# Performance work log

Measured on AMD Instinct MI355X. Metric: run time of the kernel, lower is better.

The kernel has to match this reference:

```python
import jax, jax.numpy as jnp
import numpy as np

SIDES, LAYERS, NH = 2, 2, 2
DEPTH, B = 7, 8
NPT = (3 ** DEPTH - 1) // 2  # 1093 nodes per perfect ternary tree
N = B * NPT                  # 8744
E, H = 256, 512
NUM_USERS, NUM_POIS, NUM_CATS, NUM_COOS, TMAX = 2000, 5000, 300, 50, 600
FUSE = NUM_POIS + NUM_CATS + NUM_COOS


def setup_inputs() -> dict:
    key = jax.random.key(0)
    cnt = [0]
    def nk():
        cnt[0] += 1
        return jax.random.fold_in(key, cnt[0])
    def rn(*s):
        return jax.random.normal(nk(), s, jnp.float32) * 0.02
    inp = dict(
        user_ids=jax.random.randint(nk(), (SIDES, N), 0, NUM_USERS, jnp.int32),
        feat_ids=jax.random.randint(nk(), (SIDES, N), 0, FUSE, jnp.int32),
        time_ids=jax.random.randint(nk(), (SIDES, N), 0, TMAX, jnp.int32),
        mask=jnp.ones((SIDES, N), jnp.int32),
        depth=DEPTH, n_trees=B,
        user_emb=rn(SIDES, NUM_USERS, 128), fuse_emb=rn(SIDES, FUSE, 128),
        time_pe=rn(SIDES, TMAX, E),
        Wf=rn(SIDES, H, E), bf=jnp.zeros((SIDES, H)),
        Wiou=rn(SIDES, 3 * H, E), Uiou=rn(SIDES, 3 * H, 3 * H), biou=jnp.zeros((SIDES, 3 * H)),
        attn_in_w=rn(SIDES, LAYERS, 3 * H, H), attn_in_b=jnp.zeros((SIDES, LAYERS, 3 * H)),
        attn_out_w=rn(SIDES, LAYERS, H, H), attn_out_b=jnp.zeros((SIDES, LAYERS, H)),
        ff1_w=rn(SIDES, LAYERS, H, H), ff1_b=jnp.zeros((SIDES, LAYERS, H)),
        ff2_w=rn(SIDES, LAYERS, H, H), ff2_b=jnp.zeros((SIDES, LAYERS, H)),
        ln1_w=jnp.ones((SIDES, LAYERS, H)), ln1_b=jnp.zeros((SIDES, LAYERS, H)),
        ln2_w=jnp.ones((SIDES, LAYERS, H)), ln2_b=jnp.zeros((SIDES, LAYERS, H)),
        dec_poi_w=rn(SIDES, NUM_POIS, H), dec_poi_b=jnp.zeros((SIDES, NUM_POIS)),
        dec_cat_w=rn(SIDES, NUM_CATS, H), dec_cat_b=jnp.zeros((SIDES, NUM_CATS)),
        dec_coo_w=rn(SIDES, NUM_COOS, H), dec_coo_b=jnp.zeros((SIDES, NUM_COOS)),
        cat2poi_w=rn(SIDES, NUM_POIS, NUM_CATS), cat2poi_b=jnp.zeros((SIDES, NUM_POIS)),
        coo2poi_w=rn(SIDES, NUM_POIS, NUM_COOS), coo2poi_b=jnp.zeros((SIDES, NUM_POIS)),
        mtl=jnp.ones((SIDES, 3)),
        c0=(jax.random.uniform(nk(), (SIDES, N, H), jnp.float32) * 2.0 - 1.0) * 0.025,
    )
    return inp


def _ln(x, w, b, eps=1e-5):
    m = x.mean(-1, keepdims=True)
    v = ((x - m) ** 2).mean(-1, keepdims=True)
    return (x - m) / jnp.sqrt(v + eps) * w + b


def _mha(x, iw, ib, ow, ob):
    M, S, Hd = x.shape
    q, k, v = jnp.split(x @ iw.T + ib, 3, -1)
    hd = Hd // NH
    def rs(t):
        return t.reshape(M, S, NH, hd).transpose(0, 2, 1, 3)
    q, k, v = rs(q), rs(k), rs(v)
    att = jax.nn.softmax((q * (hd ** -0.5)) @ k.transpose(0, 1, 3, 2), -1)
    o = (att @ v).transpose(0, 2, 1, 3).reshape(M, S, Hd)
    return o @ ow.T + ob


def _enc(x, iw, ib, ow, ob, f1w, f1b, f2w, f2b, l1w, l1b, l2w, l2b):
    # post-norm TransformerEncoderLayer, relu, eval mode (no dropout)
    x = _ln(x + _mha(x, iw, ib, ow, ob), l1w, l1b)
    return _ln(x + (jax.nn.relu(x @ f1w.T + f1b) @ f2w.T + f2b), l2w, l2b)


def _forward(user_ids, feat_ids, time_ids, mask, depth, n_trees,
             user_emb, fuse_emb, time_pe, Wf, bf, Wiou, Uiou, biou,
             attn_in_w, attn_in_b, attn_out_w, attn_out_b,
             ff1_w, ff1_b, ff2_w, ff2_b, ln1_w, ln1_b, ln2_w, ln2_b,
             dec_poi_w, dec_poi_b, dec_cat_w, dec_cat_b, dec_coo_w, dec_coo_b,
             cat2poi_w, cat2poi_b, coo2poi_w, coo2poi_b, mtl, c0):
    Hd = Wf.shape[1]
    npt = (3 ** depth - 1) // 2
    Bt = n_trees
    offs = [(3 ** l - 1) // 2 for l in range(depth)]
    outs = []
    for s in range(SIDES):
        m = mask[s]
        uid, fid, tid = user_ids[s] * m, feat_ids[s] * m, time_ids[s] * m
        emb = jnp.concatenate([user_emb[s][uid], fuse_emb[s][fid]], -1) + 0.5 * time_pe[s][tid]
        mf = m.astype(emb.dtype)[:, None]
        x = (emb * mf).reshape(Bt, npt, -1)              # masked node features
        iou0 = ((emb @ Wiou[s].T) * mf).reshape(Bt, npt, 3 * Hd)  # leaf iou init
        c0s = c0[s].reshape(Bt, npt, Hd)
        h = jnp.zeros((Bt, npt, Hd), emb.dtype)
        c = jnp.zeros((Bt, npt, Hd), emb.dtype)
        for l in range(depth - 1, -1, -1):  # bottom-up topo propagation, level-major layout
            st, n = offs[l], 3 ** l
            if l == depth - 1:  # leaves: no reduce, apply with initial iou and c
                iou = iou0[:, st:st + n]
                cpre = c0s[:, st:st + n]
            else:
                cs = offs[l + 1]
                hch = h[:, cs:cs + 3 * n].reshape(Bt * n, 3, Hd)   # mailbox h_child
                cch = c[:, cs:cs + 3 * n].reshape(Bt, n, 3, Hd)    # mailbox c_child
                z = hch
                for L in range(LAYERS):
                    z = _enc(z, attn_in_w[s, L], attn_in_b[s, L], attn_out_w[s, L], attn_out_b[s, L],
                             ff1_w[s, L], ff1_b[s, L], ff2_w[s, L], ff2_b[s, L],
                             ln1_w[s, L], ln1_b[s, L], ln2_w[s, L], ln2_b[s, L])
                hc = z.reshape(Bt, n, 3 * Hd)
                xl = x[:, st:st + n]
                Wx = xl @ Wf[s].T
                f = jax.nn.sigmoid(jnp.concatenate([Wx] * 3, -1) + hc + jnp.tile(bf[s], 3))
                iou = xl @ Wiou[s].T + hc @ Uiou[s].T + biou[s]
                cpre = jnp.sum(f.reshape(Bt, n, 3, Hd) * cch, axis=2)
            i, o, u = jnp.split(iou, 3, -1)
            cn = jax.nn.sigmoid(i) * jnp.tanh(u) + cpre
            hn = jax.nn.sigmoid(o) * jnp.tanh(cn)
            h = h.at[:, st:st + n].set(hn)
            c = c.at[:, st:st + n].set(cn)
        hN = h.reshape(-1, Hd)
        poi = hN @ dec_poi_w[s].T + dec_poi_b[s]
        cat = hN @ dec_cat_w[s].T + dec_cat_b[s]
        coo = hN @ dec_coo_w[s].T + dec_coo_b[s]
        p = mtl[s]
        poi_mt = (0.5 * jnp.exp(-p[0]) * poi + p[0]
                  + 0.5 * jnp.exp(-p[1]) * (cat @ cat2poi_w[s].T + cat2poi_b[s]) + p[1]
                  + 0.5 * jnp.exp(-p[2]) * (coo @ coo2poi_w[s].T + coo2poi_b[s]) + p[2])
        outs += [poi_mt, cat, coo]
    return tuple(outs)


def reference(user_ids, feat_ids, time_ids, mask, depth, n_trees,
              user_emb, fuse_emb, time_pe, Wf, bf, Wiou, Uiou, biou,
              attn_in_w, attn_in_b, attn_out_w, attn_out_b,
              ff1_w, ff1_b, ff2_w, ff2_b, ln1_w, ln1_b, ln2_w, ln2_b,
              dec_poi_w, dec_poi_b, dec_cat_w, dec_cat_b, dec_coo_w, dec_coo_b,
              cat2poi_w, cat2poi_b, coo2poi_w, coo2poi_b, mtl, c0):
    return _forward(user_ids, feat_ids, time_ids, mask, depth, n_trees,
                    user_emb, fuse_emb, time_pe, Wf, bf, Wiou, Uiou, biou,
                    attn_in_w, attn_in_b, attn_out_w, attn_out_b,
                    ff1_w, ff1_b, ff2_w, ff2_b, ln1_w, ln1_b, ln2_w, ln2_b,
                    dec_poi_w, dec_poi_b, dec_cat_w, dec_cat_b, dec_coo_w, dec_coo_b,
                    cat2poi_w, cat2poi_b, coo2poi_w, coo2poi_b, mtl, c0)
```

## Files before the change

### kernel.cpp

```cpp
#include <hip/hip_runtime.h>
#include <math.h>

#define SIDES 2
#define LAYERS 2
#define NTREE 8
#define NPT 1093
#define NN (NTREE*NPT)
#define EE 256
#define HH 512
#define NUSERS 2000
#define NPOI 5000
#define NCAT 300
#define NCOO 50
#define FUSEN 5350
#define TMAXN 600
#define TOKMAX 5832
#define PARMAX 1944

constexpr long OUT_S   = 46780400L;
constexpr long CAT_OFF = 43720000L;
constexpr long COO_OFF = 46343200L;

constexpr long H_S    = (long)NN*HH;
constexpr long X_S    = (long)NN*EE;
constexpr long Z_S    = (long)TOKMAX*HH;
constexpr long QKV_S  = (long)TOKMAX*3*HH;
constexpr long WXI_S  = (long)PARMAX*2048;
constexpr long WEFF_S = (long)NPOI*HH;

typedef __attribute__((ext_vector_type(8))) short  bf16x8;
typedef __attribute__((ext_vector_type(8))) ushort u16x8;
typedef __attribute__((ext_vector_type(4))) ushort u16x4;
typedef __attribute__((ext_vector_type(4))) float  f32x4;

__device__ __forceinline__ float sigm(float x){ return 1.f/(1.f+expf(-x)); }
__device__ __forceinline__ ushort f2b(float f){
  union { float f; unsigned u; } v; v.f = f;
  return (ushort)((v.u + 0x7fffu + ((v.u >> 16) & 1u)) >> 16);
}
__device__ __forceinline__ float b2f(ushort u){
  union { unsigned u; float f; } v; v.u = (unsigned)u << 16; return v.f;
}

constexpr int PB_EMB  = 2*NN;
constexpr int PB_MCVT = 6494;
constexpr int PB_WCOMB= 2*2048;
constexpr int PB_BCOMB= 16;
constexpr int PB_POI  = 2*5000;
constexpr int PB_TP   = 2*512;
constexpr int PB_WEI  = 2*2500;
constexpr int PB_BEF  = 40;
constexpr int PB_TOT  = PB_EMB+PB_MCVT+PB_WCOMB+PB_BCOMB+PB_POI+PB_TP+PB_WEI+PB_BEF;

__global__ void __launch_bounds__(256) prep_k(
    const int* __restrict__ uid, const int* __restrict__ fid,
    const int* __restrict__ tids, const int* __restrict__ mask,
    const float* __restrict__ uemb, const float* __restrict__ femb,
    const float* __restrict__ tpe, ushort* __restrict__ X,
    ushort* ainW, const float* attn_in_w, ushort* aoutW, const float* attn_out_w,
    ushort* f1W, const float* ff1_w, ushort* f2W, const float* ff2_w,
    ushort* dcatW, const float* dec_cat_w, ushort* dcooW, const float* dec_coo_w,
    ushort* wcomb, const float* Wf, const float* Wiou, const float* Uiou,
    float* bcomb, const float* biou,
    ushort* c2pB, const float* cat2poi_w, ushort* o2pB, const float* coo2poi_w,
    ushort* dctT, ushort* dcoT,
    ushort* weffB, const float* dec_poi_w, const float* mtl,
    float* beff, const float* dec_poi_b, const float* dec_cat_b,
    const float* cat2poi_b, const float* dec_coo_b, const float* coo2poi_b){
  int b = blockIdx.x;
  int tid = threadIdx.x;
  if (b < PB_EMB){
    int s = b / NN; long i = b - s*NN; int d = tid;
    int m = mask[(long)s*NN + i];
    int u = uid[(long)s*NN + i]*m, f = fid[(long)s*NN + i]*m, t = tids[(long)s*NN + i]*m;
    float e = (d < 128) ? uemb[((long)s*NUSERS + u)*128 + d]
                        : femb[((long)s*FUSEN + f)*128 + (d-128)];
    e += 0.5f * tpe[((long)s*TMAXN + t)*256 + d];
    X[(long)s*X_S + i*EE + d] = f2b(e * (float)m);
    return;
  }
  b -= PB_EMB;
  if (b < PB_MCVT){
    const long n0 = 3145728, n1 = 1048576, n2 = 1048576, n3 = 1048576,
               n4 = 307200, n5 = 51200;
    long i = ((long)b*256 + tid)*4;
    ushort* d; const float* s; long off;
    if      (i < n0){ d=ainW;  s=attn_in_w;  off=i; }
    else if ((i-=n0) < n1){ d=aoutW; s=attn_out_w; off=i; }
    else if ((i-=n1) < n2){ d=f1W;  s=ff1_w;  off=i; }
    else if ((i-=n2) < n3){ d=f2W;  s=ff2_w;  off=i; }
    else if ((i-=n3) < n4){ d=dcatW; s=dec_cat_w; off=i; }
    else if ((i-=n4) < n5){ d=dcooW; s=dec_coo_w; off=i; }
    else return;
    f32x4 v = *(const f32x4*)(s + off);
    *(u16x4*)(d + off) = (u16x4){f2b(v[0]), f2b(v[1]), f2b(v[2]), f2b(v[3])};
    return;
  }
  b -= PB_MCVT;
  if (b < PB_WCOMB){
    int s = b >> 11; int row = b & 2047;
    ushort* dst = wcomb + (long)s*2048*1792 + (long)row*1792;
    for (int col = tid; col < 1792; col += 256){
      float v;
      if (row < 512) v = (col < 256) ? Wf[((long)s*512 + row)*256 + col] : 0.f;
      else {
        int r = row - 512;
        v = (col < 256) ? Wiou[((long)s*1536 + r)*256 + col]
                        : Uiou[((long)s*1536 + r)*1536 + (col-256)];
      }
      dst[col] = f2b(v);
    }
    return;
  }
  b -= PB_WCOMB;
  if (b < PB_BCOMB){
    int s = b >> 3; int c = (b & 7)*256 + tid;
    bcomb[(long)s*2048 + c] = (c < 512) ? 0.f : biou[(long)s*1536 + (c-512)];
    return;
  }
  b -= PB_BCOMB;
  if (b < PB_POI){
    int s = b / 5000; int r = b - s*5000;
    for (int c = tid; c < 320; c += 256){
      float v = (c < 300) ? cat2poi_w[((long)s*5000 + r)*300 + c] : 0.f;
      c2pB[((long)s*5000 + r)*320 + c] = f2b(v);
    }
    if (tid < 64){
      float v = (tid < 50) ? coo2poi_w[((long)s*5000 + r)*50 + tid] : 0.f;
      o2pB[((long)s*5000 + r)*64 + tid] = f2b(v);
    }
    return;
  }
  b -= PB_POI;
  if (b < PB_TP){
    int s = b >> 9; int h = b & 511;
    for (int c = tid; c < 320; c += 256){
      float v = (c < 300) ? dec_cat_w[((long)s*300 + c)*512 + h] : 0.f;
      dctT[((long)s*512 + h)*320 + c] = f2b(v);
    }
    if (tid < 64){
      float v = (tid < 50) ? dec_coo_w[((long)s*50 + tid)*512 + h] : 0.f;
      dcoT[((long)s*512 + h)*64 + tid] = f2b(v);
    }
    return;
  }
  b -= PB_TP;
  if (b < PB_WEI){
    int s = b / 2500; int blk = b - s*2500;
    long i = ((long)blk*256 + tid)*4;
    float a0 = 0.5f*expf(-mtl[(long)s*3]);
    f32x4 v = *(const f32x4*)(dec_poi_w + (long)s*WEFF_S + i);
    *(u16x4*)(weffB + (long)s*WEFF_S + i) =
        (u16x4){f2b(a0*v[0]), f2b(a0*v[1]), f2b(a0*v[2]), f2b(a0*v[3])};
    return;
  }
  b -= PB_WEI;
  {
    int s = b / 20; int n = (b - s*20)*256 + tid;
    if (n >= NPOI) return;
    const float* mt = mtl + (long)s*3;
    float a0 = 0.5f*expf(-mt[0]), a1 = 0.5f*expf(-mt[1]), a2 = 0.5f*expf(-mt[2]);
    float acc1 = 0.f, acc2 = 0.f;
    for (int c = 0; c < NCAT; c++)
      acc1 += dec_cat_b[(long)s*NCAT + c] * cat2poi_w[((long)s*NPOI + n)*NCAT + c];
    for (int c = 0; c < NCOO; c++)
      acc2 += dec_coo_b[(long)s*NCOO + c] * coo2poi_w[((long)s*NPOI + n)*NCOO + c];
    beff[(long)s*NPOI + n] = a0*dec_poi_b[(long)s*NPOI + n]
        + a1*(acc1 + cat2poi_b[(long)s*NPOI + n]) + a2*(acc2 + coo2poi_b[(long)s*NPOI + n])
        + mt[0] + mt[1] + mt[2];
  }
}

template<int MODE, bool OBF>
__global__ void __launch_bounds__(256)
mgemm_k(const ushort* __restrict__ A1, long lda1, long sA1,
        const ushort* __restrict__ A2, long lda2, long sA2,
        int kSplit, int mapN, int mapOff,
        const ushort* __restrict__ Wt, long ldw, long sW,
        const float* __restrict__ bias, long sB,
        void* __restrict__ Cv, long ldc, long sC,
        int M, int Nc, int K, int nbx,
        const float* __restrict__ mtl, int mtlIdx){
  int s = blockIdx.z;
  A1 += (long)s*sA1; A2 += (long)s*sA2; Wt += (long)s*sW;
  if (bias) bias += (long)s*sB;

  int flat = blockIdx.x, nwg = gridDim.x;
  int xcd = flat & 7, q = nwg >> 3, r8 = nwg & 7;
  int nf = (xcd < r8 ? xcd*(q+1) : r8*(q+1) + (xcd - r8)*q) + (flat >> 3);
  int bx = nf % nbx, by = nf / nbx;
  int m0 = by*128, n0 = bx*128;

  __shared__ ushort As[128*64];
  __shared__ ushort Ws[128*64];

  int tid = threadIdx.x;
  int lane = tid & 63, wave = tid >> 6;
  int wr = wave >> 1, wc = wave & 1;
  int fr = lane & 15, kc = lane >> 4;

  int baseRow = tid >> 3;
  int c16 = tid & 7;
  int col8 = c16*8;
  int swz = (baseRow & 7) << 4;

  long gA1[4], gA2[4], gW[4];
  int wbyte[4];
  #pragma unroll
  for (int c = 0; c < 4; c++){
    int row = baseRow + c*32;
    int ra = m0 + row; if (ra > M-1) ra = M-1;
    gA2[c] = ra;
    if (mapN > 0){ int tr = ra / mapN; gA1[c] = (long)(tr*NPT + mapOff + (ra - tr*mapN)); }
    else gA1[c] = ra;
    int rw = n0 + row; if (rw > Nc-1) rw = Nc-1;
    gW[c] = rw;
    wbyte[c] = row*128 + ((c16*16) ^ swz);
  }

  u16x8 rA[4], rW[4];
  {
    bool u1 = (0 < kSplit);
    const ushort* asrc = u1 ? A1 : A2;
    long ld = u1 ? lda1 : lda2;
    const long* g = u1 ? gA1 : gA2;
    #pragma unroll
    for (int c = 0; c < 4; c++){
      rA[c] = *(const u16x8*)(asrc + g[c]*ld + col8);
      rW[c] = *(const u16x8*)(Wt + gW[c]*ldw + col8);
    }
  }

  f32x4 acc[4][4];
  #pragma unroll
  for (int i = 0; i < 4; i++)
    #pragma unroll
    for (int j = 0; j < 4; j++) acc[i][j] = (f32x4){0.f,0.f,0.f,0.f};

  for (int k0 = 0; k0 < K; k0 += 64){
    #pragma unroll
    for (int c = 0; c < 4; c++){
      *(u16x8*)((char*)As + wbyte[c]) = rA[c];
      *(u16x8*)((char*)Ws + wbyte[c]) = rW[c];
    }
    __syncthreads();
    int kn = k0 + 64;
    if (kn < K){
      bool u1 = (kn < kSplit);
      const ushort* asrc = u1 ? A1 : A2;
      long ld = u1 ? lda1 : lda2;
      const long* g = u1 ? gA1 : gA2;
      long colb = u1 ? (long)kn : (long)(kn - kSplit);
      #pragma unroll
      for (int c = 0; c < 4; c++){
        rA[c] = *(const u16x8*)(asrc + g[c]*ld + colb + col8);
        rW[c] = *(const u16x8*)(Wt + gW[c]*ldw + kn + col8);
      }
    }
    #pragma unroll
    for (int h = 0; h < 2; h++){
      bf16x8 af[4], bw[4];
      #pragma unroll
      for (int i = 0; i < 4; i++){
        int row = wr*64 + i*16 + fr;
        int byo = row*128 + ((h*64 + kc*16) ^ ((row & 7) << 4));
        af[i] = *(const bf16x8*)((const char*)As + byo);
      }
      #pragma unroll
      for (int j = 0; j < 4; j++){
        int row = wc*64 + j*16 + fr;
        int byo = row*128 + ((h*64 + kc*16) ^ ((row & 7) << 4));
        bw[j] = *(const bf16x8*)((const char*)Ws + byo);
      }
      #pragma unroll
      for (int i = 0; i < 4; i++)
        #pragma unroll
        for (int j = 0; j < 4; j++)
          acc[i][j] = __builtin_amdgcn_mfma_f32_16x16x32_bf16(bw[j], af[i], acc[i][j], 0, 0, 0);
    }
    __syncthreads();
  }

  float alpha = 1.f;
  if (MODE == 4) alpha = 0.5f*expf(-mtl[(long)s*3 + mtlIdx]);
  int ccol = lane & 15, cr4 = (lane >> 4)*4;
  bool vecN = ((Nc & 3) == 0);
  float* Cf = (float*)Cv + (long)s*sC;
  ushort* Cb = (ushort*)Cv + (long)s*sC;
  #pragma unroll
  for (int i = 0; i < 4; i++){
    int gm = m0 + wr*64 + i*16 + ccol;
    if (gm >= M) continue;
    long rowoff = (long)gm*ldc;
    #pragma unroll
    for (int j = 0; j < 4; j++){
      int gn0 = n0 + wc*64 + j*16 + cr4;
      if (gn0 >= Nc) continue;
      f32x4 v = acc[i][j];
      if (MODE != 4 && bias){ f32x4 bv = *(const f32x4*)&bias[gn0]; v += bv; }
      if (MODE == 1){ v = (f32x4){fmaxf(v[0],0.f),fmaxf(v[1],0.f),fmaxf(v[2],0.f),fmaxf(v[3],0.f)}; }
      if (OBF){
        u16x4* cp = (u16x4*)&Cb[rowoff + gn0];
        if (MODE == 4){
          u16x4 o = *cp;
          *cp = (u16x4){f2b(b2f(o[0]) + alpha*v[0]), f2b(b2f(o[1]) + alpha*v[1]),
                        f2b(b2f(o[2]) + alpha*v[2]), f2b(b2f(o[3]) + alpha*v[3])};
        } else {
          *cp = (u16x4){f2b(v[0]), f2b(v[1]), f2b(v[2]), f2b(v[3])};
        }
      } else {
        if (vecN){
          f32x4* cp = (f32x4*)&Cf[rowoff + gn0];
          if (MODE == 4){ f32x4 o = *cp; *cp = o + alpha*v; }
          else *cp = v;
        } else {
          #pragma unroll
          for (int r = 0; r < 4; r++){
            int gn = gn0 + r; if (gn >= Nc) continue;
            if (MODE == 4) Cf[rowoff + gn] += alpha*v[r];
            else Cf[rowoff + gn] = v[r];
          }
        }
      }
    }
  }
}

__global__ void __launch_bounds__(256) attn_k(const ushort* __restrict__ qkv,
                                              ushort* __restrict__ o){
  int s = blockIdx.z;
  int w = threadIdx.x >> 6, lane = threadIdx.x & 63;
  int seq = blockIdx.x*2 + (w >> 1);
  int h = w & 1;
  const ushort* base = qkv + (long)s*QKV_S + (long)seq*3*1536 + h*256 + lane*4;
  float q[3][4], k[3][4], v[3][4];
  #pragma unroll
  for (int i = 0; i < 3; i++){
    u16x4 tq = *(const u16x4*)(base + (long)i*1536);
    u16x4 tk = *(const u16x4*)(base + (long)i*1536 + 512);
    u16x4 tv = *(const u16x4*)(base + (long)i*1536 + 1024);
    #pragma unroll
    for (int e = 0; e < 4; e++){ q[i][e]=b2f(tq[e]); k[i][e]=b2f(tk[e]); v[i][e]=b2f(tv[e]); }
  }
  float p[9];
  #pragma unroll
  for (int i = 0; i < 3; i++)
    #pragma unroll
    for (int j = 0; j < 3; j++){
      float acc = 0.f;
      #pragma unroll
      for (int e = 0; e < 4; e++) acc += q[i][e]*k[j][e];
      p[i*3+j] = acc;
    }
  #pragma unroll
  for (int m = 1; m < 64; m <<= 1)
    #pragma unroll
    for (int t = 0; t < 9; t++) p[t] += __shfl_xor(p[t], m);
  float att[9];
  #pragma unroll
  for (int i = 0; i < 3; i++){
    float a = p[i*3]*0.0625f, bb = p[i*3+1]*0.0625f, c = p[i*3+2]*0.0625f;
    float mx = fmaxf(a, fmaxf(bb, c));
    a = expf(a-mx); bb = expf(bb-mx); c = expf(c-mx);
    float inv = 1.f/(a+bb+c);
    att[i*3] = a*inv; att[i*3+1] = bb*inv; att[i*3+2] = c*inv;
  }
  ushort* ob = o + (long)s*Z_S + (long)seq*1536 + h*256 + lane*4;
  #pragma unroll
  for (int i = 0; i < 3; i++){
    u16x4 r;
    #pragma unroll
    for (int e = 0; e < 4; e++)
      r[e] = f2b(att[i*3]*v[0][e] + att[i*3+1]*v[1][e] + att[i*3+2]*v[2][e]);
    *(u16x4*)(ob + (long)i*512) = r;
  }
}

__global__ void __launch_bounds__(256) add_ln_k(ushort* __restrict__ zout, long sZ,
                         const ushort* __restrict__ res, long sR, int mapN, int mapOff,
                         const ushort* __restrict__ tb, long sT,
                         const float* __restrict__ w, const float* __restrict__ b,
                         long wstr){
  int s = blockIdx.z;
  int wv = threadIdx.x >> 6, lane = threadIdx.x & 63;
  int r = blockIdx.x*4 + wv;
  int g = r;
  if (mapN > 0){ int tr = r / mapN; g = tr*NPT + mapOff + (r - tr*mapN); }
  int d0 = lane*8;
  u16x8 rr = *(const u16x8*)(res + (long)s*sR + (long)g*HH + d0);
  u16x8 tt = *(const u16x8*)(tb  + (long)s*sT + (long)r*HH + d0);
  float x[8];
  float sum = 0.f;
  #pragma unroll
  for (int e = 0; e < 8; e++){ x[e] = b2f(rr[e]) + b2f(tt[e]); sum += x[e]; }
  #pragma unroll
  for (int m = 1; m < 64; m <<= 1) sum += __shfl_xor(sum, m);
  float mean = sum * (1.f/512.f);
  float vs = 0.f;
  #pragma unroll
  for (int e = 0; e < 8; e++){ float d = x[e]-mean; vs += d*d; }
  #pragma unroll
  for (int m = 1; m < 64; m <<= 1) vs += __shfl_xor(vs, m);
  float inv = 1.f/sqrtf(vs*(1.f/512.f) + 1e-5f);
  const float* wr_ = w + (long)s*wstr + d0;
  const float* br_ = b + (long)s*wstr + d0;
  f32x4 w0 = *(const f32x4*)wr_, w1 = *(const f32x4*)(wr_+4);
  f32x4 b0 = *(const f32x4*)br_, b1 = *(const f32x4*)(br_+4);
  u16x8 ov;
  #pragma unroll
  for (int e = 0; e < 4; e++){
    ov[e]   = f2b((x[e]-mean)*inv*w0[e] + b0[e]);
    ov[e+4] = f2b((x[e+4]-mean)*inv*w1[e] + b1[e]);
  }
  *(u16x8*)(zout + (long)s*sZ + (long)r*HH + d0) = ov;
}

__global__ void leaf_k(const ushort* __restrict__ iou, const float* __restrict__ c0,
                       ushort* __restrict__ hbuf, float* __restrict__ cbuf){
  int s = blockIdx.z, p = blockIdx.x;
  int tree = p / 729, j = p - tree*729;
  long row = (long)(tree*NPT + 364 + j)*HH;
  const ushort* iour = iou + (long)s*QKV_S + (long)p*1536;
  const float* c0r = c0 + (long)s*H_S + row;
  for (int d = threadIdx.x; d < HH; d += 256){
    float cn = sigm(b2f(iour[d])) * tanhf(b2f(iour[1024 + d])) + c0r[d];
    float hn = sigm(b2f(iour[512 + d])) * tanhf(cn);
    hbuf[(long)s*H_S + row + d] = f2b(hn);
    cbuf[(long)s*H_S + row + d] = cn;
  }
}

__global__ void combine_k(const ushort* __restrict__ wxiou, const ushort* __restrict__ z,
                          const float* __restrict__ bfv, const float* __restrict__ cbuf,
                          ushort* __restrict__ hbuf, float* __restrict__ cout,
                          int n, int st, int cs){
  int s = blockIdx.z, p = blockIdx.x;
  int tree = p / n, j = p - tree*n;
  const ushort* wr_ = wxiou + (long)s*WXI_S + (long)p*2048;
  const ushort* zr  = z + (long)s*Z_S + (long)p*1536;
  const float* bfr  = bfv + (long)s*HH;
  const float* cch  = cbuf + (long)s*H_S + (long)(tree*NPT + cs + 3*j)*HH;
  long orow = (long)s*H_S + (long)(tree*NPT + st + j)*HH;
  for (int d = threadIdx.x; d < HH; d += 256){
    float wv = b2f(wr_[d]) + bfr[d];
    float cpre = 0.f;
    #pragma unroll
    for (int ch = 0; ch < 3; ch++){
      float fg = sigm(wv + b2f(zr[ch*512 + d]));
      cpre += fg * cch[ch*512 + d];
    }
    float iv = b2f(wr_[512 + d]), ov = b2f(wr_[1024 + d]), uv = b2f(wr_[1536 + d]);
    float cn = sigm(iv)*tanhf(uv) + cpre;
    float hn = sigm(ov)*tanhf(cn);
    hbuf[orow + d] = f2b(hn);
    cout[orow + d] = cn;
  }
}

#define GEMM(MODE, OBF, A1, LDA1, SA1, A2, LDA2, SA2, KSPL, MAPN, MAPOFF, WT, LDW, SW, \
             BI, SB, CC, LDC, SC, M, NC, K)                                            \
  do { int nbx_ = ((NC)+127)/128, nby_ = ((M)+127)/128;                                \
    mgemm_k<MODE, OBF><<<dim3(nbx_*nby_, 1, SIDES), 256, 0, stream>>>(                 \
      A1, LDA1, SA1, A2, LDA2, SA2, KSPL, MAPN, MAPOFF, WT, LDW, SW, BI, SB,           \
      CC, LDC, SC, M, NC, K, nbx_, mtl, 0); } while(0)
#define GEMM4(OBF, A1, LDA1, SA1, WT, LDW, SW, CC, LDC, SC, M, NC, K, IDX)             \
  do { int nbx_ = ((NC)+127)/128, nby_ = ((M)+127)/128;                                \
    mgemm_k<4, OBF><<<dim3(nbx_*nby_, 1, SIDES), 256, 0, stream>>>(                    \
      A1, LDA1, SA1, A1, LDA1, SA1, K, 0, 0, WT, LDW, SW, (const float*)nullptr, 0L,   \
      CC, LDC, SC, M, NC, K, nbx_, mtl, IDX); } while(0)

extern "C" void kernel_launch(void* const* d_in, const int* in_sizes, int n_in,
                              void* d_out, int out_size, void* d_ws, size_t ws_size,
                              hipStream_t stream){
  (void)in_sizes; (void)n_in; (void)out_size; (void)ws_size;
  const int*   user_ids  = (const int*)d_in[0];
  const int*   feat_ids  = (const int*)d_in[1];
  const int*   time_ids  = (const int*)d_in[2];
  const int*   mask      = (const int*)d_in[3];
  const float* user_emb  = (const float*)d_in[6];
  const float* fuse_emb  = (const float*)d_in[7];
  const float* time_pe   = (const float*)d_in[8];
  const float* Wf        = (const float*)d_in[9];
  const float* bf        = (const float*)d_in[10];
  const float* Wiou      = (const float*)d_in[11];
  const float* Uiou      = (const float*)d_in[12];
  const float* biou      = (const float*)d_in[13];
  const float* attn_in_w = (const float*)d_in[14];
  const float* attn_in_b = (const float*)d_in[15];
  const float* attn_out_w= (const float*)d_in[16];
  const float* attn_out_b= (const float*)d_in[17];
  const float* ff1_w     = (const float*)d_in[18];
  const float* ff1_b     = (const float*)d_in[19];
  const float* ff2_w     = (const float*)d_in[20];
  const float* ff2_b     = (const float*)d_in[21];
  const float* ln1_w     = (const float*)d_in[22];
  const float* ln1_b     = (const float*)d_in[23];
  const float* ln2_w     = (const float*)d_in[24];
  const float* ln2_b     = (const float*)d_in[25];
  const float* dec_poi_w = (const float*)d_in[26];
  const float* dec_poi_b = (const float*)d_in[27];
  const float* dec_cat_w = (const float*)d_in[28];
  const float* dec_cat_b = (const float*)d_in[29];
  const float* dec_coo_w = (const float*)d_in[30];
  const float* dec_coo_b = (const float*)d_in[31];
  const float* cat2poi_w = (const float*)d_in[32];
  const float* cat2poi_b = (const float*)d_in[33];
  const float* coo2poi_w = (const float*)d_in[34];
  const float* coo2poi_b = (const float*)d_in[35];
  const float* mtl       = (const float*)d_in[36];
  const float* c0        = (const float*)d_in[37];

  float* out = (float*)d_out;

  ushort* wsu = (ushort*)d_ws;
  ushort* Hb    = wsu;
  ushort* ainW  = Hb    + 2*H_S;
  ushort* aoutW = ainW  + (long)2*2*1536*512;
  ushort* f1W   = aoutW + (long)2*2*512*512;
  ushort* f2W   = f1W   + (long)2*2*512*512;
  ushort* wcomb = f2W   + (long)2*2*512*512;
  ushort* dcatW = wcomb + (long)2*2048*1792;
  ushort* dcooW = dcatW + (long)2*300*512;
  ushort* weffB = dcooW + (long)2*50*512;
  float*  bcomb = (float*)(weffB + (long)2*WEFF_S);
  float*  beff  = bcomb + 2*2048;

  float*  Cb   = out + OUT_S;
  ushort* osu  = (ushort*)(Cb + 2*H_S);
  ushort* QKV  = osu;
  ushort* Zb   = QKV  + 2*QKV_S;
  ushort* TMP  = Zb   + 2*Z_S;
  ushort* WXI  = TMP  + 2*Z_S;
  ushort* Xb   = WXI  + 2*WXI_S;
  ushort* c2pB = Xb   + 2*X_S;
  ushort* o2pB = c2pB + (long)2*5000*320;
  ushort* dctT = o2pB + (long)2*5000*64;
  ushort* dcoT = dctT + (long)2*512*320;

  prep_k<<<dim3(PB_TOT), 256, 0, stream>>>(
      user_ids, feat_ids, time_ids, mask, user_emb, fuse_emb, time_pe, Xb,
      ainW, attn_in_w, aoutW, attn_out_w, f1W, ff1_w, f2W, ff2_w,
      dcatW, dec_cat_w, dcooW, dec_coo_w,
      wcomb, Wf, Wiou, Uiou, bcomb, biou,
      c2pB, cat2poi_w, o2pB, coo2poi_w, dctT, dcoT,
      weffB, dec_poi_w, mtl,
      beff, dec_poi_b, dec_cat_b, cat2poi_b, dec_coo_b, coo2poi_b);

  GEMM(0, true, Xb, 256L, X_S, Xb, 256L, X_S, 256, 729, 364,
       wcomb + (long)512*1792, 1792L, (long)2048*1792,
       (const float*)nullptr, 0L, QKV, 1536L, QKV_S, 5832, 1536, 256);
  leaf_k<<<dim3(5832, 1, SIDES), 256, 0, stream>>>(QKV, c0, Hb, Cb);

  const int p3[7]   = {1,3,9,27,81,243,729};
  const int offs[7] = {0,1,4,13,40,121,364};

  for (int l = 5; l >= 0; l--){
    int n = p3[l], st = offs[l], cs = offs[l+1];
    int P = NTREE*n, T = 3*P;
    for (int L = 0; L < LAYERS; L++){
      const ushort* zin = (L == 0) ? Hb : Zb;
      long zld = 512, zs = (L == 0) ? H_S : Z_S;
      int mN = (L == 0) ? 3*n : 0, mO = (L == 0) ? cs : 0;
      GEMM(0, true, zin, zld, zs, zin, zld, zs, 512, mN, mO,
           ainW + (long)L*1536*512, 512L, (long)2*1536*512,
           attn_in_b + (long)L*1536, (long)LAYERS*1536, QKV, 1536L, QKV_S, T, 1536, 512);
      attn_k<<<dim3(P/2, 1, SIDES), 256, 0, stream>>>(QKV, TMP);
      GEMM(0, true, TMP, 512L, Z_S, TMP, 512L, Z_S, 512, 0, 0,
           aoutW + (long)L*512*512, 512L, (long)2*512*512,
           attn_out_b + (long)L*512, (long)LAYERS*512, QKV, 512L, QKV_S, T, 512, 512);
      add_ln_k<<<dim3(T/4, 1, SIDES), 256, 0, stream>>>(Zb, Z_S, zin, zs, mN, mO,
           QKV, QKV_S, ln1_w + (long)L*512, ln1_b + (long)L*512, (long)LAYERS*512);
      GEMM(1, true, Zb, 512L, Z_S, Zb, 512L, Z_S, 512, 0, 0,
           f1W + (long)L*512*512, 512L, (long)2*512*512,
           ff1_b + (long)L*512, (long)LAYERS*512, TMP, 512L, Z_S, T, 512, 512);
      GEMM(0, true, TMP, 512L, Z_S, TMP, 512L, Z_S, 512, 0, 0,
           f2W + (long)L*512*512, 512L, (long)2*512*512,
           ff2_b + (long)L*512, (long)LAYERS*512, QKV, 512L, QKV_S, T, 512, 512);
      add_ln_k<<<dim3(T/4, 1, SIDES), 256, 0, stream>>>(Zb, Z_S, Zb, Z_S, 0, 0,
           QKV, QKV_S, ln2_w + (long)L*512, ln2_b + (long)L*512, (long)LAYERS*512);
    }
    GEMM(0, true, Xb, 256L, X_S, Zb, 1536L, Z_S, 256, n, st,
         wcomb, 1792L, (long)2048*1792, bcomb, 2048L, WXI, 2048L, WXI_S, P, 2048, 1792);
    combine_k<<<dim3(P, 1, SIDES), 256, 0, stream>>>(WXI, Zb, bf, Cb, Hb, Cb, n, st, cs);
  }

  GEMM(0, false, Hb, 512L, H_S, Hb, 512L, H_S, 512, 0, 0,
       dcatW, 512L, (long)NCAT*512, dec_cat_b, (long)NCAT,
       out + CAT_OFF, (long)NCAT, OUT_S, NN, NCAT, 512);
  GEMM(0, false, Hb, 512L, H_S, Hb, 512L, H_S, 512, 0, 0,
       dcooW, 512L, (long)NCOO*512, dec_coo_b, (long)NCOO,
       out + COO_OFF, (long)NCOO, OUT_S, NN, NCOO, 512);

  GEMM4(true, c2pB, 320L, (long)5000*320, dctT, 320L, (long)512*320,
        weffB, 512L, WEFF_S, 5000, 512, 320, 1);
  GEMM4(true, o2pB, 64L, (long)5000*64, dcoT, 64L, (long)512*64,
        weffB, 512L, WEFF_S, 5000, 512, 64, 2);

  GEMM(0, false, Hb, 512L, H_S, Hb, 512L, H_S, 512, 0, 0,
       weffB, 512L, WEFF_S, beff, (long)NPOI,
       out, (long)NPOI, OUT_S, NN, NPOI, 512);
}
```

Baseline: 1.560 ms.

## Fuse output GEMM with residual LayerNorm for small levels; merge decoder weight-fold GEMMs

Adds a gemmln_k kernel that computes a 64-row x 512-column GEMM tile, adds bias and residual, and applies LayerNorm in shared memory. It replaces the attention-out and FF2 GEMM plus add_ln_k pairs when the token count is small (T<=648). This removes a launch and a round trip through global memory at the small tree levels that are bound by launch count and latency. Separately, the two MODE-4 accumulate GEMMs that fold cat2poi/coo2poi into the POI decoder weights become one K-concatenated GEMM, with the mtl scale pre-applied during prep. The fused kernel runs few blocks and uses a large shared-memory footprint, which limits parallelism.

```diff
diff --git a/kernel.cpp b/kernel.cpp
--- a/kernel.cpp
+++ b/kernel.cpp
@@ -63,7 +63,7 @@
     ushort* wcomb, const float* Wf, const float* Wiou, const float* Uiou,
     float* bcomb, const float* biou,
     ushort* c2pB, const float* cat2poi_w, ushort* o2pB, const float* coo2poi_w,
-    ushort* dctT, ushort* dcoT,
+    ushort* dcT2,
     ushort* weffB, const float* dec_poi_w, const float* mtl,
     float* beff, const float* dec_poi_b, const float* dec_cat_b,
     const float* cat2poi_b, const float* dec_coo_b, const float* coo2poi_b){
@@ -121,12 +121,14 @@
   b -= PB_BCOMB;
   if (b < PB_POI){
     int s = b / 5000; int r = b - s*5000;
+    float a1 = 0.5f*expf(-mtl[(long)s*3 + 1]);
+    float a2 = 0.5f*expf(-mtl[(long)s*3 + 2]);
     for (int c = tid; c < 320; c += 256){
-      float v = (c < 300) ? cat2poi_w[((long)s*5000 + r)*300 + c] : 0.f;
+      float v = (c < 300) ? a1*cat2poi_w[((long)s*5000 + r)*300 + c] : 0.f;
       c2pB[((long)s*5000 + r)*320 + c] = f2b(v);
     }
     if (tid < 64){
-      float v = (tid < 50) ? coo2poi_w[((long)s*5000 + r)*50 + tid] : 0.f;
+      float v = (tid < 50) ? a2*coo2poi_w[((long)s*5000 + r)*50 + tid] : 0.f;
       o2pB[((long)s*5000 + r)*64 + tid] = f2b(v);
     }
     return;
@@ -134,13 +136,12 @@
   b -= PB_POI;
   if (b < PB_TP){
     int s = b >> 9; int h = b & 511;
-    for (int c = tid; c < 320; c += 256){
-      float v = (c < 300) ? dec_cat_w[((long)s*300 + c)*512 + h] : 0.f;
-      dctT[((long)s*512 + h)*320 + c] = f2b(v);
-    }
-    if (tid < 64){
-      float v = (tid < 50) ? dec_coo_w[((long)s*50 + tid)*512 + h] : 0.f;
-      dcoT[((long)s*512 + h)*64 + tid] = f2b(v);
+    ushort* dst = dcT2 + ((long)s*512 + h)*384;
+    for (int c = tid; c < 384; c += 256){
+      float v = 0.f;
+      if (c < 300)                 v = dec_cat_w[((long)s*300 + c)*512 + h];
+      else if (c >= 320 && c < 370) v = dec_coo_w[((long)s*50 + (c-320))*512 + h];
+      dst[c] = f2b(v);
     }
     return;
   }
@@ -297,14 +298,15 @@
       int gn0 = n0 + wc*64 + j*16 + cr4;
       if (gn0 >= Nc) continue;
       f32x4 v = acc[i][j];
-      if (MODE != 4 && bias){ f32x4 bv = *(const f32x4*)&bias[gn0]; v += bv; }
+      if (MODE != 4 && MODE != 2 && bias){ f32x4 bv = *(const f32x4*)&bias[gn0]; v += bv; }
       if (MODE == 1){ v = (f32x4){fmaxf(v[0],0.f),fmaxf(v[1],0.f),fmaxf(v[2],0.f),fmaxf(v[3],0.f)}; }
       if (OBF){
         u16x4* cp = (u16x4*)&Cb[rowoff + gn0];
-        if (MODE == 4){
+        if (MODE == 4 || MODE == 2){
           u16x4 o = *cp;
-          *cp = (u16x4){f2b(b2f(o[0]) + alpha*v[0]), f2b(b2f(o[1]) + alpha*v[1]),
-                        f2b(b2f(o[2]) + alpha*v[2]), f2b(b2f(o[3]) + alpha*v[3])};
+          float a = (MODE == 4) ? alpha : 1.f;
+          *cp = (u16x4){f2b(b2f(o[0]) + a*v[0]), f2b(b2f(o[1]) + a*v[1]),
+                        f2b(b2f(o[2]) + a*v[2]), f2b(b2f(o[3]) + a*v[3])};
         } else {
           *cp = (u16x4){f2b(v[0]), f2b(v[1]), f2b(v[2]), f2b(v[3])};
         }
@@ -312,16 +314,171 @@
         if (vecN){
           f32x4* cp = (f32x4*)&Cf[rowoff + gn0];
           if (MODE == 4){ f32x4 o = *cp; *cp = o + alpha*v; }
+          else if (MODE == 2){ f32x4 o = *cp; *cp = o + v; }
           else *cp = v;
         } else {
           #pragma unroll
           for (int r = 0; r < 4; r++){
             int gn = gn0 + r; if (gn >= Nc) continue;
             if (MODE == 4) Cf[rowoff + gn] += alpha*v[r];
+            else if (MODE == 2) Cf[rowoff + gn] += v[r];
             else Cf[rowoff + gn] = v[r];
           }
         }
       }
+    }
+  }
+}
+
+__global__ void __launch_bounds__(256)
+gemmln_k(const ushort* __restrict__ A, long sA,
+         const ushort* __restrict__ res, long sR, int mapN, int mapOff,
+         const ushort* __restrict__ Wt, long sW,
+         const float* __restrict__ bias, long sB,
+         const float* __restrict__ lnw, const float* __restrict__ lnb, long wstr,
+         ushort* __restrict__ Zo, long sZ, int M){
+  int s = blockIdx.z;
+  A += (long)s*sA; res += (long)s*sR; Wt += (long)s*sW;
+  bias += (long)s*sB; lnw += (long)s*wstr; lnb += (long)s*wstr;
+  ushort* Z = Zo + (long)s*sZ;
+  int m0 = blockIdx.x*64;
+
+  __shared__ ushort As[64*64];
+  __shared__ ushort Ws[128*64];
+  __shared__ ushort zs[64*512];
+  __shared__ float ssum[64], ssq[64];
+
+  int tid = threadIdx.x;
+  int lane = tid & 63, wave = tid >> 6;
+  int wr = wave >> 1, wc = wave & 1;
+  int fr = lane & 15, kc = lane >> 4;
+  int ccol = lane & 15, cr4 = (lane >> 4)*4;
+
+  int baseRow = tid >> 3;
+  int c16 = tid & 7;
+  int col8 = c16*8;
+
+  long gA[2]; int abyte[2];
+  #pragma unroll
+  for (int c = 0; c < 2; c++){
+    int row = baseRow + c*32;
+    int ra = m0 + row; if (ra > M-1) ra = M-1;
+    gA[c] = ra;
+    abyte[c] = row*128 + ((c16*16) ^ ((row & 7) << 4));
+  }
+  int wbyte[4];
+  #pragma unroll
+  for (int c = 0; c < 4; c++){
+    int row = baseRow + c*32;
+    wbyte[c] = row*128 + ((c16*16) ^ ((row & 7) << 4));
+  }
+
+  float psum[2] = {0.f, 0.f}, psq[2] = {0.f, 0.f};
+
+  for (int nt = 0; nt < 4; nt++){
+    f32x4 acc[2][4];
+    #pragma unroll
+    for (int i = 0; i < 2; i++)
+      #pragma unroll
+      for (int j = 0; j < 4; j++) acc[i][j] = (f32x4){0.f,0.f,0.f,0.f};
+    for (int k0 = 0; k0 < 512; k0 += 64){
+      #pragma unroll
+      for (int c = 0; c < 2; c++)
+        *(u16x8*)((char*)As + abyte[c]) = *(const u16x8*)(A + gA[c]*512 + k0 + col8);
+      #pragma unroll
+      for (int c = 0; c < 4; c++){
+        int rw = nt*128 + baseRow + c*32;
+        *(u16x8*)((char*)Ws + wbyte[c]) = *(const u16x8*)(Wt + (long)rw*512 + k0 + col8);
+      }
+      __syncthreads();
+      #pragma unroll
+      for (int h = 0; h < 2; h++){
+        bf16x8 af[2], bw[4];
+        #pragma unroll
+        for (int i = 0; i < 2; i++){
+          int row = wr*32 + i*16 + fr;
+          int byo = row*128 + ((h*64 + kc*16) ^ ((row & 7) << 4));
+          af[i] = *(const bf16x8*)((const char*)As + byo);
+        }
+        #pragma unroll
+        for (int j = 0; j < 4; j++){
+          int row = wc*64 + j*16 + fr;
+          int byo = row*128 + ((h*64 + kc*16) ^ ((row & 7) << 4));
+          bw[j] = *(const bf16x8*)((const char*)Ws + byo);
+        }
+        #pragma unroll
+        for (int i = 0; i < 2; i++)
+          #pragma unroll
+          for (int j = 0; j < 4; j++)
+            acc[i][j] = __builtin_amdgcn_mfma_f32_16x16x32_bf16(bw[j], af[i], acc[i][j], 0, 0, 0);
+      }
+      __syncthreads();
+    }
+    #pragma unroll
+    for (int i = 0; i < 2; i++){
+      int lrow = wr*32 + i*16 + ccol;
+      int gm = m0 + lrow;
+      long g = gm;
+      if (mapN > 0){ int tr = gm / mapN; g = (long)(tr*NPT + mapOff + (gm - tr*mapN)); }
+      if (g > 0){}
+      #pragma unroll
+      for (int j = 0; j < 4; j++){
+        int gnl = wc*64 + j*16 + cr4;
+        int gn = nt*128 + gnl;
+        f32x4 v = acc[i][j];
+        f32x4 bv = *(const f32x4*)&bias[gn];
+        u16x4 rv = (gm < M) ? *(const u16x4*)(res + g*512 + gn)
+                            : (u16x4){0,0,0,0};
+        u16x4 zvec;
+        #pragma unroll
+        for (int r = 0; r < 4; r++){
+          float z = v[r] + bv[r] + b2f(rv[r]);
+          psum[i] += z; psq[i] += z*z;
+          zvec[r] = f2b(z);
+        }
+        int zbyte = lrow*1024 + ((gn*2) ^ ((lrow & 7) << 4));
+        *(u16x4*)((char*)zs + zbyte) = zvec;
+      }
+    }
+  }
+  #pragma unroll
+  for (int i = 0; i < 2; i++){
+    psum[i] += __shfl_xor(psum[i], 16); psum[i] += __shfl_xor(psum[i], 32);
+    psq[i]  += __shfl_xor(psq[i], 16);  psq[i]  += __shfl_xor(psq[i], 32);
+  }
+  __syncthreads();
+  if (wc == 0 && lane < 16){
+    #pragma unroll
+    for (int i = 0; i < 2; i++){
+      ssum[wr*32 + i*16 + lane] = psum[i];
+      ssq [wr*32 + i*16 + lane] = psq[i];
+    }
+  }
+  __syncthreads();
+  if (wc == 1 && lane < 16){
+    #pragma unroll
+    for (int i = 0; i < 2; i++){
+      ssum[wr*32 + i*16 + lane] += psum[i];
+      ssq [wr*32 + i*16 + lane] += psq[i];
+    }
+  }
+  __syncthreads();
+  int row = tid >> 2;
+  int gm = m0 + row;
+  if (gm < M){
+    float mean = ssum[row] * (1.f/512.f);
+    float var  = ssq[row] * (1.f/512.f) - mean*mean;
+    float inv  = 1.f/sqrtf(var + 1e-5f);
+    int colbase = (tid & 3)*128;
+    for (int cc = 0; cc < 16; cc++){
+      int col = colbase + cc*8;
+      int zbyte = row*1024 + ((col*2) ^ ((row & 7) << 4));
+      u16x8 zv = *(const u16x8*)((const char*)zs + zbyte);
+      u16x8 ov;
+      #pragma unroll
+      for (int e = 0; e < 8; e++)
+        ov[e] = f2b((b2f(zv[e]) - mean)*inv*lnw[col+e] + lnb[col+e]);
+      *(u16x8*)(Z + (long)gm*512 + col) = ov;
     }
   }
 }
@@ -463,11 +620,6 @@
     mgemm_k<MODE, OBF><<<dim3(nbx_*nby_, 1, SIDES), 256, 0, stream>>>(                 \
       A1, LDA1, SA1, A2, LDA2, SA2, KSPL, MAPN, MAPOFF, WT, LDW, SW, BI, SB,           \
       CC, LDC, SC, M, NC, K, nbx_, mtl, 0); } while(0)
-#define GEMM4(OBF, A1, LDA1, SA1, WT, LDW, SW, CC, LDC, SC, M, NC, K, IDX)             \
-  do { int nbx_ = ((NC)+127)/128, nby_ = ((M)+127)/128;                                \
-    mgemm_k<4, OBF><<<dim3(nbx_*nby_, 1, SIDES), 256, 0, stream>>>(                    \
-      A1, LDA1, SA1, A1, LDA1, SA1, K, 0, 0, WT, LDW, SW, (const float*)nullptr, 0L,   \
-      CC, LDC, SC, M, NC, K, nbx_, mtl, IDX); } while(0)
 
 extern "C" void kernel_launch(void* const* d_in, const int* in_sizes, int n_in,
                               void* d_out, int out_size, void* d_ws, size_t ws_size,
@@ -534,15 +686,14 @@
   ushort* Xb   = WXI  + 2*WXI_S;
   ushort* c2pB = Xb   + 2*X_S;
   ushort* o2pB = c2pB + (long)2*5000*320;
-  ushort* dctT = o2pB + (long)2*5000*64;
-  ushort* dcoT = dctT + (long)2*512*320;
+  ushort* dcT2 = o2pB + (long)2*5000*64;
 
   prep_k<<<dim3(PB_TOT), 256, 0, stream>>>(
       user_ids, feat_ids, time_ids, mask, user_emb, fuse_emb, time_pe, Xb,
       ainW, attn_in_w, aoutW, attn_out_w, f1W, ff1_w, f2W, ff2_w,
       dcatW, dec_cat_w, dcooW, dec_coo_w,
       wcomb, Wf, Wiou, Uiou, bcomb, biou,
-      c2pB, cat2poi_w, o2pB, coo2poi_w, dctT, dcoT,
+      c2pB, cat2poi_w, o2pB, coo2poi_w, dcT2,
       weffB, dec_poi_w, mtl,
       beff, dec_poi_b, dec_cat_b, cat2poi_b, dec_coo_b, coo2poi_b);
 
@@ -557,27 +708,46 @@
   for (int l = 5; l >= 0; l--){
     int n = p3[l], st = offs[l], cs = offs[l+1];
     int P = NTREE*n, T = 3*P;
+    bool fused = (T <= 648);
     for (int L = 0; L < LAYERS; L++){
       const ushort* zin = (L == 0) ? Hb : Zb;
-      long zld = 512, zs = (L == 0) ? H_S : Z_S;
+      long zs = (L == 0) ? H_S : Z_S;
       int mN = (L == 0) ? 3*n : 0, mO = (L == 0) ? cs : 0;
-      GEMM(0, true, zin, zld, zs, zin, zld, zs, 512, mN, mO,
+      GEMM(0, true, zin, 512L, zs, zin, 512L, zs, 512, mN, mO,
            ainW + (long)L*1536*512, 512L, (long)2*1536*512,
            attn_in_b + (long)L*1536, (long)LAYERS*1536, QKV, 1536L, QKV_S, T, 1536, 512);
       attn_k<<<dim3(P/2, 1, SIDES), 256, 0, stream>>>(QKV, TMP);
-      GEMM(0, true, TMP, 512L, Z_S, TMP, 512L, Z_S, 512, 0, 0,
-           aoutW + (long)L*512*512, 512L, (long)2*512*512,
-           attn_out_b + (long)L*512, (long)LAYERS*512, QKV, 512L, QKV_S, T, 512, 512);
-      add_ln_k<<<dim3(T/4, 1, SIDES), 256, 0, stream>>>(Zb, Z_S, zin, zs, mN, mO,
-           QKV, QKV_S, ln1_w + (long)L*512, ln1_b + (long)L*512, (long)LAYERS*512);
+      if (fused){
+        gemmln_k<<<dim3((T+63)/64, 1, SIDES), 256, 0, stream>>>(
+            TMP, Z_S, zin, zs, mN, mO,
+            aoutW + (long)L*512*512, (long)2*512*512,
+            attn_out_b + (long)L*512, (long)LAYERS*512,
+            ln1_w + (long)L*512, ln1_b + (long)L*512, (long)LAYERS*512,
+            Zb, Z_S, T);
+      } else {
+        GEMM(0, true, TMP, 512L, Z_S, TMP, 512L, Z_S, 512, 0, 0,
+             aoutW + (long)L*512*512, 512L, (long)2*512*512,
+             attn_out_b + (long)L*512, (long)LAYERS*512, QKV, 512L, QKV_S, T, 512, 512);
+        add_ln_k<<<dim3(T/4, 1, SIDES), 256, 0, stream>>>(Zb, Z_S, zin, zs, mN, mO,
+             QKV, QKV_S, ln1_w + (long)L*512, ln1_b + (long)L*512, (long)LAYERS*512);
+      }
       GEMM(1, true, Zb, 512L, Z_S, Zb, 512L, Z_S, 512, 0, 0,
            f1W + (long)L*512*512, 512L, (long)2*512*512,
            ff1_b + (long)L*512, (long)LAYERS*512, TMP, 512L, Z_S, T, 512, 512);
-      GEMM(0, true, TMP, 512L, Z_S, TMP, 512L, Z_S, 512, 0, 0,
-           f2W + (long)L*512*512, 512L, (long)2*512*512,
-           ff2_b + (long)L*512, (long)LAYERS*512, QKV, 512L, QKV_S, T, 512, 512);
-      add_ln_k<<<dim3(T/4, 1, SIDES), 256, 0, stream>>>(Zb, Z_S, Zb, Z_S, 0, 0,
-           QKV, QKV_S, ln2_w + (long)L*512, ln2_b + (long)L*512, (long)LAYERS*512);
+      if (fused){
+        gemmln_k<<<dim3((T+63)/64, 1, SIDES), 256, 0, stream>>>(
+            TMP, Z_S, Zb, Z_S, 0, 0,
+            f2W + (long)L*512*512, (long)2*512*512,
+            ff2_b + (long)L*512, (long)LAYERS*512,
+            ln2_w + (long)L*512, ln2_b + (long)L*512, (long)LAYERS*512,
+            Zb, Z_S, T);
+      } else {
+        GEMM(0, true, TMP, 512L, Z_S, TMP, 512L, Z_S, 512, 0, 0,
+             f2W + (long)L*512*512, 512L, (long)2*512*512,
+             ff2_b + (long)L*512, (long)LAYERS*512, QKV, 512L, QKV_S, T, 512, 512);
+        add_ln_k<<<dim3(T/4, 1, SIDES), 256, 0, stream>>>(Zb, Z_S, Zb, Z_S, 0, 0,
+             QKV, QKV_S, ln2_w + (long)L*512, ln2_b + (long)L*512, (long)LAYERS*512);
+      }
     }
     GEMM(0, true, Xb, 256L, X_S, Zb, 1536L, Z_S, 256, n, st,
          wcomb, 1792L, (long)2048*1792, bcomb, 2048L, WXI, 2048L, WXI_S, P, 2048, 1792);
@@ -591,10 +761,9 @@
        dcooW, 512L, (long)NCOO*512, dec_coo_b, (long)NCOO,
        out + COO_OFF, (long)NCOO, OUT_S, NN, NCOO, 512);
 
-  GEMM4(true, c2pB, 320L, (long)5000*320, dctT, 320L, (long)512*320,
-        weffB, 512L, WEFF_S, 5000, 512, 320, 1);
-  GEMM4(true, o2pB, 64L, (long)5000*64, dcoT, 64L, (long)512*64,
-        weffB, 512L, WEFF_S, 5000, 512, 64, 2);
+  GEMM(2, true, c2pB, 320L, (long)5000*320, o2pB, 64L, (long)5000*64, 320, 0, 0,
+       dcT2, 384L, (long)512*384, (const float*)nullptr, 0L,
+       weffB, 512L, WEFF_S, 5000, 512, 384);
 
   GEMM(0, false, Hb, 512L, H_S, Hb, 512L, H_S, 512, 0, 0,
        weffB, 512L, WEFF_S, beff, (long)NPOI,
```

New measurement: 1.931 ms. 1.24x slower.
